# Kernel tuning notes

Hardware: AMD Instinct MI355X
Metric: run time of the kernel (lower is better)

## Reference

```python
import jax, jax.numpy as jnp
import numpy as np

NUM_EMBEDDINGS = 8192
EMBEDDING_DIM = 256
COMMITMENT_COST = 0.25
TEMP = 1.0
EPS_NORM = 1e-12  # torch F.normalize eps


def setup_inputs() -> dict:
    key = jax.random.key(0)
    k1, k2 = jax.random.split(key)
    inputs = jax.random.normal(k1, (16, EMBEDDING_DIM, 32, 32), dtype=jnp.float32)
    emb_weight = jax.random.normal(k2, (NUM_EMBEDDINGS, EMBEDDING_DIM), dtype=jnp.float32) * (1.0 / NUM_EMBEDDINGS)
    return {"inputs": inputs, "emb_weight": emb_weight}


def _l2norm(x):
    n = jnp.sqrt(jnp.sum(x * x, axis=1, keepdims=True))
    return x / jnp.maximum(n, EPS_NORM)


def reference(inputs, emb_weight):
    B, C, H, W = inputs.shape
    K = emb_weight.shape[0]
    x = jnp.transpose(inputs, (0, 2, 3, 1))            # [B,H,W,C]
    flat_x = x.reshape(-1, C)                           # [N,C]
    N = flat_x.shape[0]

    # compute_distances (on L2-normalized vectors), done under no_grad in torch
    fn = _l2norm(flat_x)
    wn = _l2norm(emb_weight)
    distances = (jnp.sum(fn * fn, axis=1, keepdims=True)
                 + jnp.sum(wn * wn, axis=1)
                 - 2.0 * fn @ wn.T)                     # [N,K]

    soft_codes = jax.nn.softmax(-distances / TEMP, axis=-1)  # [N,K]
    encoding_indices = jnp.argmin(distances, axis=-1)        # [N] (stochastic=False)

    # one-hot scatter + matmul == gather of codebook rows
    quantized = emb_weight[encoding_indices].reshape(x.shape)  # [B,H,W,C]

    e_latent_loss = jnp.mean((jax.lax.stop_gradient(quantized) - x) ** 2)
    loss = COMMITMENT_COST * e_latent_loss

    # straight-through
    quantized = x + jax.lax.stop_gradient(quantized - x)
    quantized = jnp.transpose(quantized, (0, 3, 2, 1))  # [B,C,W,H] (as in source)

    # perplexity from one-hot encodings
    counts = jnp.zeros((K,), dtype=jnp.float32).at[encoding_indices].add(1.0)
    avg_probs = counts / N
    perplexity = jnp.exp(-jnp.sum(avg_probs * jnp.log(avg_probs + 1e-10)))

    soft_codes = soft_codes.reshape(B, C, -1)
    return quantized, loss, perplexity, encoding_indices[:, None], soft_codes
```

## Files before the change

kernel.cpp:

```cpp
#include <hip/hip_runtime.h>

#define NPTS   16384
#define KCB    8192
#define CDIM   256
#define HWSZ   1024
#define NB     16

typedef __bf16 bf16;
typedef __bf16 bf16x4v __attribute__((ext_vector_type(4)));
typedef __bf16 bf16x8v __attribute__((ext_vector_type(8)));
typedef float  f32x4v  __attribute__((ext_vector_type(4)));
typedef float  f32x2v  __attribute__((ext_vector_type(2)));

#define OUT1 4194304
#define OUT2 4194305
#define OUT3 4194306
#define OUT4 4210690

#define MAX_RESCUE 4096
#define ENT_INTS   16

typedef __attribute__((address_space(1))) unsigned int as1_u32;
typedef __attribute__((address_space(3))) unsigned int as3_u32;
__device__ __forceinline__ void glds16(const bf16* g, bf16* l) {
  __builtin_amdgcn_global_load_lds((as1_u32*)(g), (as3_u32*)(l), 16, 0, 0);
}

__global__ void k_norm_emb(const float* __restrict__ emb,
                           bf16* __restrict__ wn_hi, bf16* __restrict__ wn_lo) {
  const int lane = threadIdx.x & 63;
  const int row  = (blockIdx.x << 2) + (threadIdx.x >> 6);
  const float4 v = *(const float4*)(emb + (size_t)row * CDIM + (lane << 2));
  float ss = v.x*v.x + v.y*v.y + v.z*v.z + v.w*v.w;
#pragma unroll
  for (int off = 1; off < 64; off <<= 1) ss += __shfl_xor(ss, off, 64);
  const float inv = 1.0f / fmaxf(sqrtf(ss), 1e-12f);
  const float a0 = v.x*inv, a1 = v.y*inv, a2 = v.z*inv, a3 = v.w*inv;
  const bf16 h0 = (bf16)a0, h1 = (bf16)a1, h2 = (bf16)a2, h3 = (bf16)a3;
  const bf16 l0 = (bf16)(a0 - (float)h0), l1 = (bf16)(a1 - (float)h1),
             l2 = (bf16)(a2 - (float)h2), l3 = (bf16)(a3 - (float)h3);
  *(bf16x4v*)(wn_hi + (size_t)row * CDIM + (lane << 2)) = (bf16x4v){h0, h1, h2, h3};
  *(bf16x4v*)(wn_lo + (size_t)row * CDIM + (lane << 2)) = (bf16x4v){l0, l1, l2, l3};
}

__global__ void k_norm_x(const float* __restrict__ in,
                         bf16* __restrict__ fn_hi, bf16* __restrict__ fn_lo) {
  __shared__ float xs[32][257];
  __shared__ float inv_s[32];
  const int t = threadIdx.x;
  const int b = blockIdx.y;
  const int hw0 = blockIdx.x << 5;
  const int hwo = t & 31, cb = t >> 5;
  const float* src = in + (size_t)b * CDIM * HWSZ + hw0 + hwo;
#pragma unroll
  for (int it = 0; it < 32; ++it) {
    const int c = cb + (it << 3);
    xs[hwo][c] = src[(size_t)c * HWSZ];
  }
  __syncthreads();
  const int wv = t >> 6, lane = t & 63;
#pragma unroll
  for (int j = 0; j < 8; ++j) {
    const int r = wv + (j << 2);
    float ss = 0.f;
#pragma unroll
    for (int e = 0; e < 4; ++e) { const float x = xs[r][lane + (e << 6)]; ss = fmaf(x, x, ss); }
#pragma unroll
    for (int off = 1; off < 64; off <<= 1) ss += __shfl_xor(ss, off, 64);
    if (lane == 0) inv_s[r] = 1.0f / fmaxf(sqrtf(ss), 1e-12f);
  }
  __syncthreads();
#pragma unroll 4
  for (int r = 0; r < 32; ++r) {
    const float v = xs[r][t] * inv_s[r];
    const bf16 h = (bf16)v;
    const bf16 l = (bf16)(v - (float)h);
    const size_t n = (size_t)b * HWSZ + hw0 + r;
    fn_hi[n * CDIM + t] = h;
    fn_lo[n * CDIM + t] = l;
  }
}

__global__ __launch_bounds__(256) void k_gemm(
    const bf16* __restrict__ fn_hi, const bf16* __restrict__ fn_lo,
    const bf16* __restrict__ wn_hi, const bf16* __restrict__ wn_lo,
    float* __restrict__ soft) {
  __shared__ __align__(16) bf16 Ah[128 * 32];
  __shared__ __align__(16) bf16 Al[128 * 32];
  __shared__ __align__(16) bf16 Bh[128 * 32];
  __shared__ __align__(16) bf16 Bl[128 * 32];
  const int t = threadIdx.x;

  const int bid = blockIdx.x;
  const int xcd = bid & 7;
  const int g   = bid >> 3;
  const int s   = (xcd << 3) + (g >> 7);
  const int w   = g & 127;
  const int rowt = ((s >> 3) << 4) + (w >> 3);
  const int colt = ((s & 7) << 3) + (w & 7);
  const int row0 = rowt << 7;
  const int col0 = colt << 7;

  const int r0 = t >> 2;
  const int cs = (t & 3) << 3;
  const int wv = t >> 6, lane = t & 63;
  const int wm = (wv & 1) << 6, wnn = (wv >> 1) << 6;
  const int ml = lane & 15, quad = lane >> 4;

  const size_t gA0 = (size_t)(row0 + r0) * CDIM + cs;
  const size_t gA1 = gA0 + (size_t)64 * CDIM;
  const size_t gB0 = (size_t)(col0 + r0) * CDIM + cs;
  const size_t gB1 = gB0 + (size_t)64 * CDIM;

  f32x4v acc[4][4] = {};

  for (int c0 = 0; c0 < CDIM; c0 += 32) {
    __syncthreads();
    glds16(fn_hi + gA0 + c0, Ah + t * 8);
    glds16(fn_hi + gA1 + c0, Ah + (t + 256) * 8);
    glds16(fn_lo + gA0 + c0, Al + t * 8);
    glds16(fn_lo + gA1 + c0, Al + (t + 256) * 8);
    glds16(wn_hi + gB0 + c0, Bh + t * 8);
    glds16(wn_hi + gB1 + c0, Bh + (t + 256) * 8);
    glds16(wn_lo + gB0 + c0, Bl + t * 8);
    glds16(wn_lo + gB1 + c0, Bl + (t + 256) * 8);
    __syncthreads();
    bf16x8v ah[4], alo[4], bh[4], blo[4];
#pragma unroll
    for (int i = 0; i < 4; ++i) {
      const int ra = (wm + 16 * i + ml) * 32 + quad * 8;
      const int rb = (wnn + 16 * i + ml) * 32 + quad * 8;
      ah[i]  = *(const bf16x8v*)(Ah + ra);
      alo[i] = *(const bf16x8v*)(Al + ra);
      bh[i]  = *(const bf16x8v*)(Bh + rb);
      blo[i] = *(const bf16x8v*)(Bl + rb);
    }
#pragma unroll
    for (int i = 0; i < 4; ++i)
#pragma unroll
      for (int j = 0; j < 4; ++j) {
        acc[i][j] = __builtin_amdgcn_mfma_f32_16x16x32_bf16(alo[i], bh[j], acc[i][j], 0, 0, 0);
        acc[i][j] = __builtin_amdgcn_mfma_f32_16x16x32_bf16(ah[i], blo[j], acc[i][j], 0, 0, 0);
        acc[i][j] = __builtin_amdgcn_mfma_f32_16x16x32_bf16(ah[i], bh[j], acc[i][j], 0, 0, 0);
      }
  }
#pragma unroll
  for (int i = 0; i < 4; ++i) {
#pragma unroll
    for (int r = 0; r < 4; ++r) {
      const size_t nrow = (size_t)row0 + wm + 16 * i + quad * 4 + r;
      float* dst = soft + nrow * KCB + col0 + wnn + ml;
#pragma unroll
      for (int j = 0; j < 4; ++j)
        __builtin_nontemporal_store(__expf(fmaf(2.0f, acc[i][j][r], -2.0f)), dst + 16 * j);
    }
  }
}

__global__ __launch_bounds__(256) void k_softnorm(float* __restrict__ soft,
                                                  int* __restrict__ ws_idx,
                                                  int* __restrict__ rescue,
                                                  int* __restrict__ rescue_cnt) {
  const int t = threadIdx.x;
  const size_t n = blockIdx.x;
  float* row = soft + n * (size_t)KCB;
  f32x2v v[16];
  float sum = 0.f, bp = -1.f;
  int bk = 0;
#pragma unroll
  for (int i = 0; i < 16; ++i) {
    v[i] = __builtin_nontemporal_load((const f32x2v*)(row + i * 512 + t * 2));
    const int k0 = i * 512 + t * 2;
    if (v[i][0] > bp) { bp = v[i][0]; bk = k0; }
    if (v[i][1] > bp) { bp = v[i][1]; bk = k0 + 1; }
    sum += v[i][0] + v[i][1];
  }
#pragma unroll
  for (int off = 1; off < 64; off <<= 1) {
    sum += __shfl_xor(sum, off, 64);
    const float op = __shfl_xor(bp, off, 64);
    const int   ok = __shfl_xor(bk, off, 64);
    if (op > bp || (op == bp && ok < bk)) { bp = op; bk = ok; }
  }
  __shared__ float s_sum[4], s_bp[4];
  __shared__ int s_bk[4];
  __shared__ int s_cand[16];
  __shared__ int s_ccnt;
  const int wv = t >> 6;
  if (t == 0) s_ccnt = 0;
  if ((t & 63) == 0) { s_sum[wv] = sum; s_bp[wv] = bp; s_bk[wv] = bk; }
  __syncthreads();
  sum = s_sum[0] + s_sum[1] + s_sum[2] + s_sum[3];
  bp = s_bp[0]; bk = s_bk[0];
#pragma unroll
  for (int w2 = 1; w2 < 4; ++w2) {
    const float op = s_bp[w2]; const int ok = s_bk[w2];
    if (op > bp || (op == bp && ok < bk)) { bp = op; bk = ok; }
  }
  const float thr = bp * (1.0f - 5e-4f);
#pragma unroll
  for (int i = 0; i < 16; ++i) {
    if (v[i][0] >= thr) { const int p = atomicAdd(&s_ccnt, 1); if (p < 16) s_cand[p] = i * 512 + t * 2; }
    if (v[i][1] >= thr) { const int p = atomicAdd(&s_ccnt, 1); if (p < 16) s_cand[p] = i * 512 + t * 2 + 1; }
  }
  __syncthreads();
  if (t == 0) {
    ws_idx[n] = bk;
    int cc = s_ccnt; if (cc > 16) cc = 16;
    if (cc > 1) {
      const int slot = atomicAdd(rescue_cnt, 1);
      if (slot < MAX_RESCUE) {
        int* e = rescue + slot * ENT_INTS;
        const int cn = cc > 14 ? 14 : cc;
        e[0] = (int)n; e[1] = cn;
        for (int j = 0; j < cn; ++j) e[2 + j] = s_cand[j];
      }
    }
  }
  const float inv = 1.0f / sum;
#pragma unroll
  for (int i = 0; i < 16; ++i) {
    v[i][0] *= inv; v[i][1] *= inv;
    __builtin_nontemporal_store(v[i], (f32x2v*)(row + i * 512 + t * 2));
  }
}

__global__ __launch_bounds__(256) void k_rescore(const float* __restrict__ in,
                                                 const float* __restrict__ emb,
                                                 const int* __restrict__ rescue,
                                                 const int* __restrict__ rescue_cnt,
                                                 int* __restrict__ ws_idx) {
  __shared__ double sh[4];
  const int t = threadIdx.x;
  int nent = *rescue_cnt; if (nent > MAX_RESCUE) nent = MAX_RESCUE;
  for (int e = blockIdx.x; e < nent; e += gridDim.x) {
    const int* ent = rescue + e * ENT_INTS;
    const int n = ent[0];
    const int cnt = ent[1];
    const int b = n >> 10, hw = n & 1023;
    const double x = (double)in[(size_t)b * (CDIM * HWSZ) + (size_t)t * HWSZ + hw];
    double sx = x * x;
#pragma unroll
    for (int off = 1; off < 64; off <<= 1) sx += __shfl_xor(sx, off, 64);
    if ((t & 63) == 0) sh[t >> 6] = sx;
    __syncthreads();
    sx = sh[0] + sh[1] + sh[2] + sh[3];
    __syncthreads();
    const double xin = 1.0 / fmax(sqrt(sx), 1e-12);
    double bestS = -2.0; int bestk = 0x7fffffff;
    for (int j = 0; j < cnt; ++j) {
      const int k = ent[2 + j];
      const double w = (double)emb[(size_t)k * CDIM + t];
      double sw = w * w, dp = x * w;
#pragma unroll
      for (int off = 1; off < 64; off <<= 1) { sw += __shfl_xor(sw, off, 64); dp += __shfl_xor(dp, off, 64); }
      if ((t & 63) == 0) sh[t >> 6] = sw;
      __syncthreads();
      sw = sh[0] + sh[1] + sh[2] + sh[3];
      __syncthreads();
      if ((t & 63) == 0) sh[t >> 6] = dp;
      __syncthreads();
      dp = sh[0] + sh[1] + sh[2] + sh[3];
      __syncthreads();
      const double s = dp * xin / fmax(sqrt(sw), 1e-12);
      if (s > bestS || (s == bestS && k < bestk)) { bestS = s; bestk = k; }
    }
    if (t == 0) ws_idx[n] = bestk;
  }
}

__global__ void k_hist(const int* __restrict__ ws_idx, float* __restrict__ counts,
                       float* __restrict__ out_idx) {
  const int n = blockIdx.x * 256 + threadIdx.x;
  const int k = ws_idx[n];
  out_idx[n] = (float)k;
  atomicAdd(&counts[k], 1.0f);
}

__global__ void k_quant(const float* __restrict__ emb, const int* __restrict__ ws_idx,
                        float* __restrict__ out0) {
  const int b = blockIdx.x >> 8, c = blockIdx.x & 255;
  const int t = threadIdx.x;
  float* dst = out0 + ((size_t)b * CDIM + c) * HWSZ;
#pragma unroll
  for (int p = t; p < HWSZ; p += 256) {
    const int w = p >> 5, h = p & 31;
    const int n = b * HWSZ + h * 32 + w;
    dst[p] = emb[(size_t)ws_idx[n] * CDIM + c];
  }
}

__global__ void k_loss(const float* __restrict__ in, const float* __restrict__ emb,
                       const int* __restrict__ ws_idx, float* __restrict__ loss_acc) {
  const int t = threadIdx.x, lane = t & 63, wv = t >> 6;
  const int b = blockIdx.x >> 4;
  const int hw = ((blockIdx.x & 15) << 6) + lane;
  const int n = b * HWSZ + hw;
  const float* xp = in + (size_t)b * CDIM * HWSZ + hw;
  const float* ep = emb + (size_t)ws_idx[n] * CDIM;
  float ss = 0.f;
#pragma unroll 8
  for (int cc = 0; cc < 64; ++cc) {
    const int c = (wv << 6) + cc;
    const float d = ep[c] - xp[(size_t)c * HWSZ];
    ss = fmaf(d, d, ss);
  }
#pragma unroll
  for (int off = 1; off < 64; off <<= 1) ss += __shfl_xor(ss, off, 64);
  if (lane == 0) atomicAdd(loss_acc, ss);
}

__global__ void k_final(const float* __restrict__ counts, const float* __restrict__ loss_acc,
                        float* __restrict__ out) {
  const int t = threadIdx.x;
  float s = 0.f;
#pragma unroll
  for (int k = t; k < KCB; k += 256) {
    const float avg = counts[k] * (1.0f / (float)NPTS);
    s += avg * logf(avg + 1e-10f);
  }
#pragma unroll
  for (int off = 1; off < 64; off <<= 1) s += __shfl_xor(s, off, 64);
  __shared__ float sw[4];
  if ((t & 63) == 0) sw[t >> 6] = s;
  __syncthreads();
  if (t == 0) {
    const float S = sw[0] + sw[1] + sw[2] + sw[3];
    out[OUT2] = expf(-S);
    out[OUT1] = 0.25f * loss_acc[0] * (1.0f / 4194304.0f);
  }
}

extern "C" void kernel_launch(void* const* d_in, const int* in_sizes, int n_in,
                              void* d_out, int out_size, void* d_ws, size_t ws_size,
                              hipStream_t stream) {
  const float* inp = (const float*)d_in[0];
  const float* emb = (const float*)d_in[1];
  float* out = (float*)d_out;
  char* ws = (char*)d_ws;

  bf16* wn_hi     = (bf16*)(ws);
  bf16* wn_lo     = (bf16*)(ws + 4194304);
  float* counts   = (float*)(ws + 8388608);
  float* loss_a   = (float*)(ws + 8421376);
  int* rescue_cnt = (int*)(ws + 8421380);
  int* ws_idx     = (int*)(ws + 8421632);
  int* rescue     = (int*)(ws + 8487168);

  bf16* fn_hi = (bf16*)out;
  bf16* fn_lo = ((bf16*)out) + (size_t)NPTS * CDIM;

  (void)hipMemsetAsync(ws + 8388608, 0, 33024, stream);
  k_norm_emb<<<KCB / 4, 256, 0, stream>>>(emb, wn_hi, wn_lo);
  k_norm_x<<<dim3(32, NB), 256, 0, stream>>>(inp, fn_hi, fn_lo);
  k_gemm<<<8192, 256, 0, stream>>>(fn_hi, fn_lo, wn_hi, wn_lo, out + OUT4);
  k_softnorm<<<NPTS, 256, 0, stream>>>(out + OUT4, ws_idx, rescue, rescue_cnt);
  k_rescore<<<256, 256, 0, stream>>>(inp, emb, rescue, rescue_cnt, ws_idx);
  k_hist<<<NPTS / 256, 256, 0, stream>>>(ws_idx, counts, out + OUT3);
  k_quant<<<NB * CDIM, 256, 0, stream>>>(emb, ws_idx, out);
  k_loss<<<256, 256, 0, stream>>>(inp, emb, ws_idx, loss_a);
  k_final<<<1, 256, 0, stream>>>(counts, loss_a, out);
}
```

Measured before the change: 982.1 us.

## Merge prep and post-quantization kernels; transpose quantized output through shared memory

Codebook normalization, input normalization and the workspace zeroing are folded into one launch. The histogram, quantized-output and loss kernels are folded into a second launch, which removes the separate memset and several kernel launches. The quantized output now gathers 8 channels per codebook row with float4 loads into a skewed shared-memory tile, then writes coalesced nontemporal stores, instead of gathering single floats per channel. The risk is that the mixed-role blocks run unevenly and that the large shared tile lowers occupancy.

```diff
diff --git a/kernel.cpp b/kernel.cpp
--- a/kernel.cpp
+++ b/kernel.cpp
@@ -26,30 +26,38 @@
   __builtin_amdgcn_global_load_lds((as1_u32*)(g), (as3_u32*)(l), 16, 0, 0);
 }
 
-__global__ void k_norm_emb(const float* __restrict__ emb,
-                           bf16* __restrict__ wn_hi, bf16* __restrict__ wn_lo) {
-  const int lane = threadIdx.x & 63;
-  const int row  = (blockIdx.x << 2) + (threadIdx.x >> 6);
-  const float4 v = *(const float4*)(emb + (size_t)row * CDIM + (lane << 2));
-  float ss = v.x*v.x + v.y*v.y + v.z*v.z + v.w*v.w;
-#pragma unroll
-  for (int off = 1; off < 64; off <<= 1) ss += __shfl_xor(ss, off, 64);
-  const float inv = 1.0f / fmaxf(sqrtf(ss), 1e-12f);
-  const float a0 = v.x*inv, a1 = v.y*inv, a2 = v.z*inv, a3 = v.w*inv;
-  const bf16 h0 = (bf16)a0, h1 = (bf16)a1, h2 = (bf16)a2, h3 = (bf16)a3;
-  const bf16 l0 = (bf16)(a0 - (float)h0), l1 = (bf16)(a1 - (float)h1),
-             l2 = (bf16)(a2 - (float)h2), l3 = (bf16)(a3 - (float)h3);
-  *(bf16x4v*)(wn_hi + (size_t)row * CDIM + (lane << 2)) = (bf16x4v){h0, h1, h2, h3};
-  *(bf16x4v*)(wn_lo + (size_t)row * CDIM + (lane << 2)) = (bf16x4v){l0, l1, l2, l3};
-}
-
-__global__ void k_norm_x(const float* __restrict__ in,
-                         bf16* __restrict__ fn_hi, bf16* __restrict__ fn_lo) {
+__global__ void k_prep(const float* __restrict__ emb,
+                       bf16* __restrict__ wn_hi, bf16* __restrict__ wn_lo,
+                       const float* __restrict__ in,
+                       bf16* __restrict__ fn_hi, bf16* __restrict__ fn_lo,
+                       float* __restrict__ zero_base) {
   __shared__ float xs[32][257];
   __shared__ float inv_s[32];
   const int t = threadIdx.x;
-  const int b = blockIdx.y;
-  const int hw0 = blockIdx.x << 5;
+  const int bid = blockIdx.x;
+  if (bid < 2048) {
+    const int lane = t & 63;
+    const int row  = (bid << 2) + (t >> 6);
+    const float4 v = *(const float4*)(emb + (size_t)row * CDIM + (lane << 2));
+    float ss = v.x*v.x + v.y*v.y + v.z*v.z + v.w*v.w;
+#pragma unroll
+    for (int off = 1; off < 64; off <<= 1) ss += __shfl_xor(ss, off, 64);
+    const float inv = 1.0f / fmaxf(sqrtf(ss), 1e-12f);
+    const float a0 = v.x*inv, a1 = v.y*inv, a2 = v.z*inv, a3 = v.w*inv;
+    const bf16 h0 = (bf16)a0, h1 = (bf16)a1, h2 = (bf16)a2, h3 = (bf16)a3;
+    const bf16 l0 = (bf16)(a0 - (float)h0), l1 = (bf16)(a1 - (float)h1),
+               l2 = (bf16)(a2 - (float)h2), l3 = (bf16)(a3 - (float)h3);
+    *(bf16x4v*)(wn_hi + (size_t)row * CDIM + (lane << 2)) = (bf16x4v){h0, h1, h2, h3};
+    *(bf16x4v*)(wn_lo + (size_t)row * CDIM + (lane << 2)) = (bf16x4v){l0, l1, l2, l3};
+    return;
+  }
+  if (bid == 2560) {
+    for (int i = t; i < 8194; i += 256) zero_base[i] = 0.0f;
+    return;
+  }
+  const int bx = bid - 2048;
+  const int b = bx >> 5;
+  const int hw0 = (bx & 31) << 5;
   const int hwo = t & 31, cb = t >> 5;
   const float* src = in + (size_t)b * CDIM * HWSZ + hw0 + hwo;
 #pragma unroll
@@ -269,45 +277,70 @@
   }
 }
 
-__global__ void k_hist(const int* __restrict__ ws_idx, float* __restrict__ counts,
-                       float* __restrict__ out_idx) {
-  const int n = blockIdx.x * 256 + threadIdx.x;
+__global__ __launch_bounds__(256) void k_postq(const float* __restrict__ emb,
+                                               const int* __restrict__ ws_idx,
+                                               float* __restrict__ out0,
+                                               const float* __restrict__ in,
+                                               float* __restrict__ loss_acc,
+                                               float* __restrict__ counts,
+                                               float* __restrict__ out_idx) {
+  __shared__ float q[1024 * 9];
+  const int t = threadIdx.x;
+  const int bid = blockIdx.x;
+  if (bid < 512) {
+    const int b = bid >> 5, cg = bid & 31;
+    const int c0 = cg << 3;
+    const int* wsi = ws_idx + b * HWSZ;
+#pragma unroll
+    for (int it = 0; it < 8; ++it) {
+      const int task = t + (it << 8);
+      const int n = task >> 1, part = task & 1;
+      const int k = wsi[n];
+      const float4 v = *(const float4*)(emb + (size_t)k * CDIM + c0 + (part << 2));
+      const int s = n >> 5;
+      float* row = q + n * 9;
+      row[((part << 2) + 0 + s) & 7] = v.x;
+      row[((part << 2) + 1 + s) & 7] = v.y;
+      row[((part << 2) + 2 + s) & 7] = v.z;
+      row[((part << 2) + 3 + s) & 7] = v.w;
+    }
+    __syncthreads();
+#pragma unroll
+    for (int co = 0; co < 8; ++co) {
+      const int c = c0 + co;
+      float* dst = out0 + ((size_t)b * CDIM + c) * HWSZ;
+#pragma unroll
+      for (int p = t; p < HWSZ; p += 256) {
+        const int n = ((p & 31) << 5) | (p >> 5);
+        __builtin_nontemporal_store(q[n * 9 + ((co + (n >> 5)) & 7)], dst + p);
+      }
+    }
+    return;
+  }
+  if (bid < 768) {
+    const int bb = bid - 512;
+    const int lane = t & 63, wv = t >> 6;
+    const int b = bb >> 4;
+    const int hw = ((bb & 15) << 6) + lane;
+    const int n = b * HWSZ + hw;
+    const float* xp = in + (size_t)b * CDIM * HWSZ + hw;
+    const float* ep = emb + (size_t)ws_idx[n] * CDIM;
+    float ss = 0.f;
+#pragma unroll 8
+    for (int cc = 0; cc < 64; ++cc) {
+      const int c = (wv << 6) + cc;
+      const float d = ep[c] - xp[(size_t)c * HWSZ];
+      ss = fmaf(d, d, ss);
+    }
+#pragma unroll
+    for (int off = 1; off < 64; off <<= 1) ss += __shfl_xor(ss, off, 64);
+    if (lane == 0) atomicAdd(loss_acc, ss);
+    return;
+  }
+  const int n = (bid - 768) * 256 + t;
   const int k = ws_idx[n];
   out_idx[n] = (float)k;
   atomicAdd(&counts[k], 1.0f);
-}
-
-__global__ void k_quant(const float* __restrict__ emb, const int* __restrict__ ws_idx,
-                        float* __restrict__ out0) {
-  const int b = blockIdx.x >> 8, c = blockIdx.x & 255;
-  const int t = threadIdx.x;
-  float* dst = out0 + ((size_t)b * CDIM + c) * HWSZ;
-#pragma unroll
-  for (int p = t; p < HWSZ; p += 256) {
-    const int w = p >> 5, h = p & 31;
-    const int n = b * HWSZ + h * 32 + w;
-    dst[p] = emb[(size_t)ws_idx[n] * CDIM + c];
-  }
-}
-
-__global__ void k_loss(const float* __restrict__ in, const float* __restrict__ emb,
-                       const int* __restrict__ ws_idx, float* __restrict__ loss_acc) {
-  const int t = threadIdx.x, lane = t & 63, wv = t >> 6;
-  const int b = blockIdx.x >> 4;
-  const int hw = ((blockIdx.x & 15) << 6) + lane;
-  const int n = b * HWSZ + hw;
-  const float* xp = in + (size_t)b * CDIM * HWSZ + hw;
-  const float* ep = emb + (size_t)ws_idx[n] * CDIM;
-  float ss = 0.f;
-#pragma unroll 8
-  for (int cc = 0; cc < 64; ++cc) {
-    const int c = (wv << 6) + cc;
-    const float d = ep[c] - xp[(size_t)c * HWSZ];
-    ss = fmaf(d, d, ss);
-  }
-#pragma unroll
-  for (int off = 1; off < 64; off <<= 1) ss += __shfl_xor(ss, off, 64);
-  if (lane == 0) atomicAdd(loss_acc, ss);
 }
 
 __global__ void k_final(const float* __restrict__ counts, const float* __restrict__ loss_acc,
@@ -350,14 +383,10 @@
   bf16* fn_hi = (bf16*)out;
   bf16* fn_lo = ((bf16*)out) + (size_t)NPTS * CDIM;
 
-  (void)hipMemsetAsync(ws + 8388608, 0, 33024, stream);
-  k_norm_emb<<<KCB / 4, 256, 0, stream>>>(emb, wn_hi, wn_lo);
-  k_norm_x<<<dim3(32, NB), 256, 0, stream>>>(inp, fn_hi, fn_lo);
+  k_prep<<<2561, 256, 0, stream>>>(emb, wn_hi, wn_lo, inp, fn_hi, fn_lo, counts);
   k_gemm<<<8192, 256, 0, stream>>>(fn_hi, fn_lo, wn_hi, wn_lo, out + OUT4);
   k_softnorm<<<NPTS, 256, 0, stream>>>(out + OUT4, ws_idx, rescue, rescue_cnt);
   k_rescore<<<256, 256, 0, stream>>>(inp, emb, rescue, rescue_cnt, ws_idx);
-  k_hist<<<NPTS / 256, 256, 0, stream>>>(ws_idx, counts, out + OUT3);
-  k_quant<<<NB * CDIM, 256, 0, stream>>>(emb, ws_idx, out);
-  k_loss<<<256, 256, 0, stream>>>(inp, emb, ws_idx, loss_a);
+  k_postq<<<832, 256, 0, stream>>>(emb, ws_idx, out, inp, loss_a, counts, out + OUT3);
   k_final<<<1, 256, 0, stream>>>(counts, loss_a, out);
 }
```

New measurement: 957.4 us. 2.5% less time.
